# Performance work log

Measured on AMD Instinct MI355X. Metric: run time of the kernel, lower is better.

## Reference

```python
import jax, jax.numpy as jnp
import numpy as np

B, T, I, H, C = 256, 2048, 64, 32, 2


def setup_inputs() -> dict:
    key = jax.random.key(0)
    ks = jax.random.split(key, 12)
    s = 0.1
    return {
        "values": jax.random.normal(ks[0], (B, T, I), dtype=jnp.float32),
        "masks": (jax.random.uniform(ks[1], (B, T, I)) > 0.5).astype(jnp.float32),
        "deltas": jax.random.uniform(ks[2], (B, T, I), dtype=jnp.float32),
        # TemporalDecay linear: input_size -> rnn_hidden_size
        "W_decay": jax.random.normal(ks[3], (H, I), dtype=jnp.float32) * s,
        "b_decay": jax.random.normal(ks[4], (H,), dtype=jnp.float32) * s,
        "W_reg": jax.random.normal(ks[5], (I, H), dtype=jnp.float32) * s,
        "b_reg": jax.random.normal(ks[6], (I,), dtype=jnp.float32) * s,
        # LSTMCell: input 2*I, hidden H; gate order i,f,g,o (PyTorch)
        "W_ih": jax.random.normal(ks[7], (4 * H, 2 * I), dtype=jnp.float32) * s,
        "b_ih": jax.random.normal(ks[8], (4 * H,), dtype=jnp.float32) * s,
        "W_hh": jax.random.normal(ks[9], (4 * H, H), dtype=jnp.float32) * s,
        "b_hh": jax.random.normal(ks[10], (4 * H,), dtype=jnp.float32) * s,
        # output head: hidden -> n_classes
        "W_out": jax.random.normal(ks[11], (C, H), dtype=jnp.float32) * s,
        "b_out": jnp.zeros((C,), dtype=jnp.float32),
    }


def reference(values, masks, deltas, W_decay, b_decay, W_reg, b_reg,
              W_ih, b_ih, W_hh, b_hh, W_out, b_out):
    batch = values.shape[0]
    hid = W_decay.shape[0]

    def step(carry, xs):
        h, c = carry
        x, m, d = xs  # each [B, I]
        # gamma = exp(-relu(W d + b)); decay hidden state
        gamma = jnp.exp(-jax.nn.relu(d @ W_decay.T + b_decay))
        h = h * gamma
        x_h = h @ W_reg.T + b_reg
        x_c = m * x + (1.0 - m) * x_h
        inp = jnp.concatenate([x_c, m], axis=1)  # [B, 2I]
        gates = inp @ W_ih.T + b_ih + h @ W_hh.T + b_hh  # [B, 4H]
        i_g, f_g, g_g, o_g = jnp.split(gates, 4, axis=1)
        i_g = jax.nn.sigmoid(i_g)
        f_g = jax.nn.sigmoid(f_g)
        g_g = jnp.tanh(g_g)
        o_g = jax.nn.sigmoid(o_g)
        c_new = f_g * c + i_g * g_g
        h_new = o_g * jnp.tanh(c_new)
        return (h_new, c_new), x_c

    h0 = jnp.zeros((batch, hid), dtype=values.dtype)
    c0 = jnp.zeros((batch, hid), dtype=values.dtype)
    xs = (jnp.swapaxes(values, 0, 1), jnp.swapaxes(masks, 0, 1), jnp.swapaxes(deltas, 0, 1))
    (h, c), x_cs = jax.lax.scan(step, (h0, c0), xs)
    imputations = jnp.swapaxes(x_cs, 0, 1)  # [B, T, I]
    y_h = h @ W_out.T + b_out  # [B, C]
    return y_h, imputations
```

## Files before the change

kernel.cpp:

```cpp
#include <hip/hip_runtime.h>
#include <stdint.h>

#define L2E 1.4426950408889634f

typedef __attribute__((ext_vector_type(8))) short short8;
typedef __attribute__((ext_vector_type(4))) float floatx4;
typedef __attribute__((ext_vector_type(4))) unsigned int uintx4;
typedef __attribute__((ext_vector_type(2))) _Float16 half2v;

__device__ __forceinline__ uint32_t pkbf(float lo, float hi) {
  uint32_t r;
  asm("v_cvt_pk_bf16_f32 %0, %1, %2" : "=v"(r) : "v"(lo), "v"(hi));
  return r;
}
__device__ __forceinline__ uint32_t pkh(float lo, float hi) {
  uint32_t r;
  asm("v_cvt_pkrtz_f16_f32 %0, %1, %2" : "=v"(r) : "v"(lo), "v"(hi));
  return r;
}
__device__ __forceinline__ float2 uph(uint32_t u) {
  union { uint32_t u; half2v h; } z; z.u = u;
  return make_float2((float)z.h.x, (float)z.h.y);
}
__device__ __forceinline__ short8 mkfrag(const float* p) {
  float4 a = *(const float4*)p;
  float4 b = *(const float4*)(p + 4);
  union { uint32_t u[4]; short8 s; } z;
  z.u[0] = pkbf(a.x, a.y); z.u[1] = pkbf(a.z, a.w);
  z.u[2] = pkbf(b.x, b.y); z.u[3] = pkbf(b.z, b.w);
  return z.s;
}
__device__ __forceinline__ short8 pk8(float4 a, float4 b) {
  union { uint32_t u[4]; short8 s; } z;
  z.u[0] = pkbf(a.x, a.y); z.u[1] = pkbf(a.z, a.w);
  z.u[2] = pkbf(b.x, b.y); z.u[3] = pkbf(b.z, b.w);
  return z.s;
}
__device__ __forceinline__ short8 u4s8(uint32_t a, uint32_t b, uint32_t c, uint32_t d) {
  union { uint32_t u[4]; short8 s; } z;
  z.u[0] = a; z.u[1] = b; z.u[2] = c; z.u[3] = d;
  return z.s;
}

#define SWAP32(a, b) asm("v_permlane32_swap_b32 %0, %1" : "+v"(a), "+v"(b))
#define SWAP16(a, b) asm("v_permlane16_swap_b32 %0, %1" : "+v"(a), "+v"(b))

__global__ __launch_bounds__(256) void g1_pre(
    const float* __restrict__ values, const float* __restrict__ masks,
    const float* __restrict__ W_ih, const float* __restrict__ b_ih,
    const float* __restrict__ b_hh, uint2* __restrict__ pregS,
    uint2* __restrict__ mxS, float* __restrict__ m1S, int gstride)
{
  const int tid = threadIdx.x, wv = tid >> 6, l = tid & 63;
  const int c = l & 15, kw = l >> 4;
  const int tch = blockIdx.x, gr = blockIdx.y;
  const int tbase = tch * 8;

  short8 WF[8][4];
  #pragma unroll
  for (int tg = 0; tg < 8; ++tg)
    #pragma unroll
    for (int kc = 0; kc < 4; ++kc)
      WF[tg][kc] = mkfrag(W_ih + (size_t)(16*tg + c)*128 + 32*kc + 8*kw);

  float4 bias[8];
  #pragma unroll
  for (int tg = 0; tg < 8; ++tg) {
    float4 bi = *(const float4*)(b_ih + 16*tg + 4*kw);
    float4 bh = *(const float4*)(b_hh + 16*tg + 4*kw);
    bias[tg] = make_float4(bi.x+bh.x, bi.y+bh.y, bi.z+bh.z, bi.w+bh.w);
  }

  #pragma unroll 1
  for (int tt = 0; tt < 2; ++tt) {
    const int rec = tbase + wv*2 + tt;
    const size_t ibase = ((size_t)(gr*16 + c)*2048 + rec)*64;
    const float* xr = values + ibase;
    const float* mr = masks + ibase;
    float4 xa0 = *(const float4*)(xr + 8*kw),      xa1 = *(const float4*)(xr + 8*kw + 4);
    float4 xb0 = *(const float4*)(xr + 32 + 8*kw), xb1 = *(const float4*)(xr + 32 + 8*kw + 4);
    float4 ma0 = *(const float4*)(mr + 8*kw),      ma1 = *(const float4*)(mr + 8*kw + 4);
    float4 mb0 = *(const float4*)(mr + 32 + 8*kw), mb1 = *(const float4*)(mr + 32 + 8*kw + 4);
    float4 fa0 = make_float4(xa0.x*ma0.x, xa0.y*ma0.y, xa0.z*ma0.z, xa0.w*ma0.w);
    float4 fa1 = make_float4(xa1.x*ma1.x, xa1.y*ma1.y, xa1.z*ma1.z, xa1.w*ma1.w);
    float4 fb0 = make_float4(xb0.x*mb0.x, xb0.y*mb0.y, xb0.z*mb0.z, xb0.w*mb0.w);
    float4 fb1 = make_float4(xb1.x*mb1.x, xb1.y*mb1.y, xb1.z*mb1.z, xb1.w*mb1.w);

    short8 BF0 = pk8(fa0, fa1), BF1 = pk8(fb0, fb1);
    short8 BF2 = pk8(ma0, ma1), BF3 = pk8(mb0, mb1);

    floatx4 acc[8];
    #pragma unroll
    for (int tg = 0; tg < 8; ++tg) acc[tg] = (floatx4){0.f, 0.f, 0.f, 0.f};
    #pragma unroll
    for (int tg = 0; tg < 8; ++tg) {
      acc[tg] = __builtin_amdgcn_mfma_f32_16x16x32_bf16(WF[tg][0], BF0, acc[tg], 0, 0, 0);
      acc[tg] = __builtin_amdgcn_mfma_f32_16x16x32_bf16(WF[tg][1], BF1, acc[tg], 0, 0, 0);
      acc[tg] = __builtin_amdgcn_mfma_f32_16x16x32_bf16(WF[tg][2], BF2, acc[tg], 0, 0, 0);
      acc[tg] = __builtin_amdgcn_mfma_f32_16x16x32_bf16(WF[tg][3], BF3, acc[tg], 0, 0, 0);
    }

    uint2* pf = pregS + (size_t)(gr*gstride + rec)*512 + (c + 16*kw);
    #pragma unroll
    for (int tg = 0; tg < 8; ++tg)
      pf[tg*64] = make_uint2(pkh(acc[tg][0]+bias[tg].x, acc[tg][1]+bias[tg].y),
                             pkh(acc[tg][2]+bias[tg].z, acc[tg][3]+bias[tg].w));

    uint2* mx2 = mxS + (size_t)(gr*gstride + rec)*256;
    mx2[(2*kw+0)*16 + c] = make_uint2(pkh(fa0.x,fa0.y), pkh(fa0.z,fa0.w));
    mx2[(2*kw+1)*16 + c] = make_uint2(pkh(fa1.x,fa1.y), pkh(fa1.z,fa1.w));
    mx2[(8+2*kw)*16 + c] = make_uint2(pkh(fb0.x,fb0.y), pkh(fb0.z,fb0.w));
    mx2[(9+2*kw)*16 + c] = make_uint2(pkh(fb1.x,fb1.y), pkh(fb1.z,fb1.w));

    float4* m14 = (float4*)m1S + (size_t)(gr*gstride + rec)*256;
    m14[(2*kw+0)*16 + c] = make_float4(1.f-ma0.x, 1.f-ma0.y, 1.f-ma0.z, 1.f-ma0.w);
    m14[(2*kw+1)*16 + c] = make_float4(1.f-ma1.x, 1.f-ma1.y, 1.f-ma1.z, 1.f-ma1.w);
    m14[(8+2*kw)*16 + c] = make_float4(1.f-mb0.x, 1.f-mb0.y, 1.f-mb0.z, 1.f-mb0.w);
    m14[(9+2*kw)*16 + c] = make_float4(1.f-mb1.x, 1.f-mb1.y, 1.f-mb1.z, 1.f-mb1.w);
  }
}

__global__ __launch_bounds__(256) void g2_gam(
    const float* __restrict__ deltas, const float* __restrict__ W_decay,
    const float* __restrict__ b_decay, float* __restrict__ gamS, int gstride)
{
  const int tid = threadIdx.x, wv = tid >> 6, l = tid & 63;
  const int c = l & 15, kw = l >> 4;
  const int tch = blockIdx.x, gr = blockIdx.y;
  const int tbase = tch * 8;

  short8 AF[2][2];
  #pragma unroll
  for (int jt = 0; jt < 2; ++jt)
    #pragma unroll
    for (int kc = 0; kc < 2; ++kc)
      AF[jt][kc] = mkfrag(W_decay + (size_t)(16*jt + c)*64 + 32*kc + 8*kw);
  float4 bd0 = *(const float4*)(b_decay + 4*kw);
  float4 bd1 = *(const float4*)(b_decay + 16 + 4*kw);

  #pragma unroll 1
  for (int tt = 0; tt < 2; ++tt) {
    const int rec = tbase + wv*2 + tt;
    const float* dr = deltas + ((size_t)(gr*16 + c)*2048 + rec)*64;
    float4 da0 = *(const float4*)(dr + 8*kw),      da1 = *(const float4*)(dr + 8*kw + 4);
    float4 db0 = *(const float4*)(dr + 32 + 8*kw), db1 = *(const float4*)(dr + 32 + 8*kw + 4);
    short8 B0 = pk8(da0, da1), B1 = pk8(db0, db1);
    floatx4 zz = (floatx4){0.f, 0.f, 0.f, 0.f};
    floatx4 a0 = __builtin_amdgcn_mfma_f32_16x16x32_bf16(AF[0][0], B0, zz, 0, 0, 0);
    a0 = __builtin_amdgcn_mfma_f32_16x16x32_bf16(AF[0][1], B1, a0, 0, 0, 0);
    floatx4 a1 = __builtin_amdgcn_mfma_f32_16x16x32_bf16(AF[1][0], B0, zz, 0, 0, 0);
    a1 = __builtin_amdgcn_mfma_f32_16x16x32_bf16(AF[1][1], B1, a1, 0, 0, 0);
    float g0 = __builtin_amdgcn_exp2f(-fmaxf(a0[0]+bd0.x, 0.f) * L2E);
    float g1 = __builtin_amdgcn_exp2f(-fmaxf(a0[1]+bd0.y, 0.f) * L2E);
    float g2 = __builtin_amdgcn_exp2f(-fmaxf(a0[2]+bd0.z, 0.f) * L2E);
    float g3 = __builtin_amdgcn_exp2f(-fmaxf(a0[3]+bd0.w, 0.f) * L2E);
    float h0 = __builtin_amdgcn_exp2f(-fmaxf(a1[0]+bd1.x, 0.f) * L2E);
    float h1 = __builtin_amdgcn_exp2f(-fmaxf(a1[1]+bd1.y, 0.f) * L2E);
    float h2 = __builtin_amdgcn_exp2f(-fmaxf(a1[2]+bd1.z, 0.f) * L2E);
    float h3 = __builtin_amdgcn_exp2f(-fmaxf(a1[3]+bd1.w, 0.f) * L2E);
    uintx4 o = (uintx4){pkh(g0, g1), pkh(g2, g3), pkh(h0, h1), pkh(h2, h3)};
    ((uintx4*)gamS)[(size_t)(gr*gstride + rec)*64 + c + 16*kw] = o;
  }
}

#define PW(GI, GF, GG, GO, CC, HH) do { \
  float _si = __builtin_amdgcn_rcpf(1.f + __builtin_amdgcn_exp2f((GI) * -L2E)); \
  float _sf = __builtin_amdgcn_rcpf(1.f + __builtin_amdgcn_exp2f((GF) * -L2E)); \
  float _so = __builtin_amdgcn_rcpf(1.f + __builtin_amdgcn_exp2f((GO) * -L2E)); \
  float _tg = 1.f - 2.f*__builtin_amdgcn_rcpf(1.f + __builtin_amdgcn_exp2f((GG) * (2.f*L2E))); \
  float _cn = fmaf(_sf, (CC), _si*_tg); \
  float _tc = 1.f - 2.f*__builtin_amdgcn_rcpf(1.f + __builtin_amdgcn_exp2f(_cn * (2.f*L2E))); \
  (CC) = _cn; (HH) = _so * _tc; \
} while (0)

__global__ __launch_bounds__(128, 1) void p13_rnn(
    const float* __restrict__ W_hh, const float* __restrict__ W_reg,
    const float* __restrict__ W_ih, const float* __restrict__ b_reg,
    const float* __restrict__ W_out, const float* __restrict__ b_out,
    const uint2* __restrict__ pregS, const char* __restrict__ gamS,
    const float* __restrict__ m1S, char* __restrict__ hdG,
    float* __restrict__ y, int gstride)
{
  const int tid = threadIdx.x, gr = blockIdx.x;
  const int wid = tid >> 6, l = tid & 63;
  const int b = l & 15, w = l >> 4;

  __shared__ __align__(16) char hdB[2 * 1536];
  __shared__ float yL[2][16][2];

  short8 WhhA[4], WxcA0[4], WxcA1[4], WregA[4];
  #pragma unroll
  for (int tt = 0; tt < 4; ++tt) {
    const int tg = 2*tt + wid;
    WhhA[tt]  = mkfrag(W_hh + (size_t)(16*tg + b)*32 + 8*w);
    WxcA0[tt] = mkfrag(W_ih + (size_t)(16*tg + b)*128 + 8*w);
    WxcA1[tt] = mkfrag(W_ih + (size_t)(16*tg + b)*128 + 32 + 8*w);
    WregA[tt] = mkfrag(W_reg + (size_t)(16*tt + b)*32 + 8*w);
  }
  floatx4 brC[4];
  #pragma unroll
  for (int t = 0; t < 4; ++t) {
    float4 v = *(const float4*)(b_reg + 16*t + 4*w);
    brC[t] = (floatx4){v.x, v.y, v.z, v.w};
  }

  float4 h = make_float4(0.f, 0.f, 0.f, 0.f);
  float4 cv = make_float4(0.f, 0.f, 0.f, 0.f);

  const uint2* pPreg = pregS + (size_t)gr*gstride*512 + l;
  const char*  gamB  = gamS + (size_t)gr*gstride*1024 + (size_t)(b + 16*w)*16 + wid*8;
  const float4* pM1  = (const float4*)m1S + (size_t)gr*gstride*256;
  char* hdP = hdG + (size_t)gr*gstride*1024 + b*64 + wid*32 + w*8;

  uint2 PR[2][4], GM[2];
  float4 M1r[2][4];

  auto PREF = [&](int s, int j) {
    #pragma unroll
    for (int tt = 0; tt < 4; ++tt) PR[j][tt] = pPreg[(size_t)s*512 + (2*tt + wid)*64];
    GM[j] = *(const uint2*)(gamB + (size_t)s*1024);
    #pragma unroll
    for (int t = 0; t < 4; ++t) M1r[j][t] = pM1[(size_t)s*256 + (4*t + w)*16 + b];
  };

  auto BODY = [&](int j, int par) {
    float2 g01 = uph(GM[j].x), g23 = uph(GM[j].y);
    float4 hd = make_float4(h.x*g01.x, h.y*g01.y, h.z*g23.x, h.w*g23.y);
    uint32_t K0 = pkbf(hd.x, hd.y), K1 = pkbf(hd.z, hd.w);
    uint32_t S0 = K0, S1 = K1;
    *(uint2*)hdP = make_uint2(S0, S1);
    hdP += 1024;
    *(uint2*)(hdB + par*1536 + b*96 + wid*32 + w*8) = make_uint2(K0, K1);
    asm volatile("s_waitcnt lgkmcnt(0)" ::: "memory");
    __builtin_amdgcn_s_barrier();
    asm volatile("" ::: "memory");
    short8 Bhd = *(const short8*)(hdB + par*1536 + b*96 + w*16);

    floatx4 uu[4];
    #pragma unroll
    for (int t = 0; t < 4; ++t)
      uu[t] = __builtin_amdgcn_mfma_f32_16x16x32_bf16(WregA[t], Bhd, brC[t], 0, 0, 0);
    floatx4 ga[4];
    #pragma unroll
    for (int tt = 0; tt < 4; ++tt) {
      float2 p01 = uph(PR[j][tt].x), p23 = uph(PR[j][tt].y);
      floatx4 ci = {p01.x, p01.y, p23.x, p23.y};
      ga[tt] = __builtin_amdgcn_mfma_f32_16x16x32_bf16(WhhA[tt], Bhd, ci, 0, 0, 0);
    }

    uint32_t U[8];
    #pragma unroll
    for (int t = 0; t < 4; ++t) {
      float4 m1v = M1r[j][t];
      float v0 = m1v.x*uu[t][0], v1 = m1v.y*uu[t][1];
      float v2 = m1v.z*uu[t][2], v3 = m1v.w*uu[t][3];
      U[2*t]   = pkbf(v0, v1);
      U[2*t+1] = pkbf(v2, v3);
    }
    SWAP32(U[0], U[2]); SWAP32(U[1], U[3]);
    SWAP16(U[0], U[2]); SWAP16(U[1], U[3]);
    short8 Bv0 = u4s8(U[0], U[1], U[2], U[3]);
    SWAP32(U[4], U[6]); SWAP32(U[5], U[7]);
    SWAP16(U[4], U[6]); SWAP16(U[5], U[7]);
    short8 Bv1 = u4s8(U[4], U[5], U[6], U[7]);

    #pragma unroll
    for (int tt = 0; tt < 4; ++tt)
      ga[tt] = __builtin_amdgcn_mfma_f32_16x16x32_bf16(WxcA0[tt], Bv0, ga[tt], 0, 0, 0);
    #pragma unroll
    for (int tt = 0; tt < 4; ++tt)
      ga[tt] = __builtin_amdgcn_mfma_f32_16x16x32_bf16(WxcA1[tt], Bv1, ga[tt], 0, 0, 0);

    PW(ga[0][0], ga[1][0], ga[2][0], ga[3][0], cv.x, h.x);
    PW(ga[0][1], ga[1][1], ga[2][1], ga[3][1], cv.y, h.y);
    PW(ga[0][2], ga[1][2], ga[2][2], ga[3][2], cv.z, h.z);
    PW(ga[0][3], ga[1][3], ga[2][3], ga[3][3], cv.w, h.w);
  };

  PREF(0, 0); PREF(1, 1);
  #pragma unroll 1
  for (int s = 0; s < 2048; s += 2) {
    BODY(0, 0); PREF(s + 2, 0);
    BODY(1, 1); PREF(s + 3, 1);
  }

  {
    auto d4 = [](float4 a, float4 bb) {
      return fmaf(a.x, bb.x, fmaf(a.y, bb.y, fmaf(a.z, bb.z, a.w*bb.w)));
    };
    float4 wo0 = *(const float4*)(W_out + wid*16 + 4*w);
    float4 wo1 = *(const float4*)(W_out + 32 + wid*16 + 4*w);
    float p0 = d4(h, wo0);
    float p1 = d4(h, wo1);
    p0 += __shfl_xor(p0, 16); p0 += __shfl_xor(p0, 32);
    p1 += __shfl_xor(p1, 16); p1 += __shfl_xor(p1, 32);
    if (l < 16) { yL[wid][l][0] = p0; yL[wid][l][1] = p1; }
    asm volatile("s_waitcnt lgkmcnt(0)" ::: "memory");
    __builtin_amdgcn_s_barrier();
    asm volatile("" ::: "memory");
    if (wid == 0 && l < 16) {
      y[(gr*16 + l)*2 + 0] = yL[0][l][0] + yL[1][l][0] + b_out[0];
      y[(gr*16 + l)*2 + 1] = yL[0][l][1] + yL[1][l][1] + b_out[1];
    }
  }
}

__global__ __launch_bounds__(256) void p13_post(
    const float* __restrict__ W_reg, const float* __restrict__ b_reg,
    const char* __restrict__ hdG, const uint2* __restrict__ mxS,
    const float* __restrict__ m1S, float* __restrict__ imp, int gstride)
{
  const int tid = threadIdx.x, wv = tid >> 6, l = tid & 63;
  const int c = l & 15, kw = l >> 4;
  const int tch = blockIdx.x, gr = blockIdx.y;
  const int tbase = tch * 8;

  short8 WA[4];
  #pragma unroll
  for (int t = 0; t < 4; ++t)
    WA[t] = mkfrag(W_reg + (size_t)(16*t + c)*32 + 8*kw);
  floatx4 brC[4];
  #pragma unroll
  for (int t = 0; t < 4; ++t) {
    float4 v = *(const float4*)(b_reg + 16*t + 4*kw);
    brC[t] = (floatx4){v.x, v.y, v.z, v.w};
  }

  #pragma unroll 1
  for (int tt = 0; tt < 2; ++tt) {
    const int rec = tbase + wv*2 + tt;
    short8 Bhd = *(const short8*)(hdG + (size_t)(gr*gstride + rec)*1024 + c*64 + kw*16);
    floatx4 uu[4];
    #pragma unroll
    for (int t = 0; t < 4; ++t)
      uu[t] = __builtin_amdgcn_mfma_f32_16x16x32_bf16(WA[t], Bhd, brC[t], 0, 0, 0);

    float* dst = imp + ((size_t)(gr*16 + c)*2048 + rec)*64 + 4*kw;
    #pragma unroll
    for (int t = 0; t < 4; ++t) {
      float4 m1v = ((const float4*)m1S)[(size_t)(gr*gstride + rec)*256 + (4*t + kw)*16 + c];
      uint2 mxv = mxS[(size_t)(gr*gstride + rec)*256 + (4*t + kw)*16 + c];
      float2 mxa = uph(mxv.x), mxb = uph(mxv.y);
      *(float4*)(dst + 16*t) = make_float4(
          fmaf(m1v.x, uu[t][0], mxa.x), fmaf(m1v.y, uu[t][1], mxa.y),
          fmaf(m1v.z, uu[t][2], mxb.x), fmaf(m1v.w, uu[t][3], mxb.y));
    }
  }
}

extern "C" void kernel_launch(void* const* d_in, const int* in_sizes, int n_in,
                              void* d_out, int out_size, void* d_ws, size_t ws_size,
                              hipStream_t stream) {
  (void)in_sizes; (void)n_in; (void)out_size; (void)ws_size;
  const float* values  = (const float*)d_in[0];
  const float* masks   = (const float*)d_in[1];
  const float* deltas  = (const float*)d_in[2];
  const float* W_decay = (const float*)d_in[3];
  const float* b_decay = (const float*)d_in[4];
  const float* W_reg   = (const float*)d_in[5];
  const float* b_reg   = (const float*)d_in[6];
  const float* W_ih    = (const float*)d_in[7];
  const float* b_ih    = (const float*)d_in[8];
  const float* W_hh    = (const float*)d_in[9];
  const float* b_hh    = (const float*)d_in[10];
  const float* W_out   = (const float*)d_in[11];
  const float* b_out   = (const float*)d_in[12];
  float* y   = (float*)d_out;
  float* imp = (float*)d_out + 512;

  const int gstride = 2056;
  char* pregS = (char*)d_ws;
  char* gamS  = pregS + (size_t)16*gstride*4096;
  char* mxS   = gamS  + (size_t)16*gstride*1024;
  char* m1S   = mxS   + (size_t)16*gstride*2048;
  char* hdG   = m1S   + (size_t)16*gstride*4096;

  hipLaunchKernelGGL(g1_pre, dim3(256, 16), dim3(256), 0, stream,
                     values, masks, W_ih, b_ih, b_hh,
                     (uint2*)pregS, (uint2*)mxS, (float*)m1S, gstride);
  hipLaunchKernelGGL(g2_gam, dim3(256, 16), dim3(256), 0, stream,
                     deltas, W_decay, b_decay, (float*)gamS, gstride);
  hipLaunchKernelGGL(p13_rnn, dim3(16), dim3(128), 0, stream,
                     W_hh, W_reg, W_ih, b_reg, W_out, b_out,
                     (const uint2*)pregS, gamS, (const float*)m1S, hdG, y, gstride);
  hipLaunchKernelGGL(p13_post, dim3(256, 16), dim3(256), 0, stream,
                     W_reg, b_reg, hdG, (const uint2*)mxS, (const float*)m1S,
                     imp, gstride);
}
```

Measured before the change: 1.614 ms.

## Stage recurrent per-step inputs through an LDS ring via async global-to-LDS loads

The serial RNN kernel now prefetches each timestep's precomputed gate pre-activations, mask products and decay factors three steps ahead. It uses global_load_lds into a 4-slot shared-memory ring instead of loading them straight into registers two steps ahead. Per-wave vmcnt waits plus the existing per-step barrier ensure each slot has landed before it is read back from LDS one step ahead. The aim is to hide global memory latency on the latency-bound recurrence and free registers, at the cost of extra LDS traffic, about 37 KB of shared memory, and delicate wait-count bookkeeping.

```diff
diff --git a/kernel.cpp b/kernel.cpp
--- a/kernel.cpp
+++ b/kernel.cpp
@@ -44,6 +44,9 @@
 
 #define SWAP32(a, b) asm("v_permlane32_swap_b32 %0, %1" : "+v"(a), "+v"(b))
 #define SWAP16(a, b) asm("v_permlane16_swap_b32 %0, %1" : "+v"(a), "+v"(b))
+#define GLDS16(gp, lp) __builtin_amdgcn_global_load_lds( \
+    (const __attribute__((address_space(1))) void*)(gp), \
+    (__attribute__((address_space(3))) void*)(lp), 16, 0, 0)
 
 __global__ __launch_bounds__(256) void g1_pre(
     const float* __restrict__ values, const float* __restrict__ masks,
@@ -173,18 +176,21 @@
   (CC) = _cn; (HH) = _so * _tc; \
 } while (0)
 
-__global__ __launch_bounds__(128, 1) void p13_rnn(
+#define SLOTB 9216
+
+__global__ __launch_bounds__(128, 1) void p14_rnn(
     const float* __restrict__ W_hh, const float* __restrict__ W_reg,
     const float* __restrict__ W_ih, const float* __restrict__ b_reg,
     const float* __restrict__ W_out, const float* __restrict__ b_out,
-    const uint2* __restrict__ pregS, const char* __restrict__ gamS,
-    const float* __restrict__ m1S, char* __restrict__ hdG,
+    const char* __restrict__ pregS, const char* __restrict__ gamS,
+    const char* __restrict__ m1S, char* __restrict__ hdG,
     float* __restrict__ y, int gstride)
 {
   const int tid = threadIdx.x, gr = blockIdx.x;
   const int wid = tid >> 6, l = tid & 63;
   const int b = l & 15, w = l >> 4;
 
+  __shared__ __align__(16) char ring[4 * SLOTB];
   __shared__ __align__(16) char hdB[2 * 1536];
   __shared__ float yL[2][16][2];
 
@@ -207,34 +213,59 @@
   float4 h = make_float4(0.f, 0.f, 0.f, 0.f);
   float4 cv = make_float4(0.f, 0.f, 0.f, 0.f);
 
-  const uint2* pPreg = pregS + (size_t)gr*gstride*512 + l;
-  const char*  gamB  = gamS + (size_t)gr*gstride*1024 + (size_t)(b + 16*w)*16 + wid*8;
-  const float4* pM1  = (const float4*)m1S + (size_t)gr*gstride*256;
+  const char* pregB = pregS + (size_t)gr*gstride*4096 + (size_t)l*16;
+  const char* gamGB = gamS  + (size_t)gr*gstride*1024 + (size_t)l*16;
+  const char* m1B   = m1S   + (size_t)gr*gstride*4096 + (size_t)l*16;
   char* hdP = hdG + (size_t)gr*gstride*1024 + b*64 + wid*32 + w*8;
 
-  uint2 PR[2][4], GM[2];
+  auto PREFL = [&](int rec, int slot) {
+    char* sb = ring + slot * SLOTB;
+    const char* pb = pregB + (size_t)rec*4096;
+    const char* mb = m1B   + (size_t)rec*4096;
+    if (wid == 0) {
+      GLDS16(pb,        sb);
+      GLDS16(pb + 1024, sb + 1024);
+      GLDS16(pb + 2048, sb + 2048);
+      GLDS16(pb + 3072, sb + 3072);
+      GLDS16(mb,        sb + 4096);
+    } else {
+      GLDS16(mb + 1024, sb + 5120);
+      GLDS16(mb + 2048, sb + 6144);
+      GLDS16(mb + 3072, sb + 7168);
+      GLDS16(gamGB + (size_t)rec*1024, sb + 8192);
+    }
+  };
+
+  uint2 PRr[2][4], GMr[2];
   float4 M1r[2][4];
 
-  auto PREF = [&](int s, int j) {
-    #pragma unroll
-    for (int tt = 0; tt < 4; ++tt) PR[j][tt] = pPreg[(size_t)s*512 + (2*tt + wid)*64];
-    GM[j] = *(const uint2*)(gamB + (size_t)s*1024);
-    #pragma unroll
-    for (int t = 0; t < 4; ++t) M1r[j][t] = pM1[(size_t)s*256 + (4*t + w)*16 + b];
+  auto LDSRD = [&](int slot, int j) {
+    const char* sb = ring + slot * SLOTB;
+    #pragma unroll
+    for (int tt = 0; tt < 4; ++tt)
+      PRr[j][tt] = *(const uint2*)(sb + ((2*tt + wid)*64 + l)*8);
+    GMr[j] = *(const uint2*)(sb + 8192 + (b + 16*w)*16 + wid*8);
+    #pragma unroll
+    for (int t = 0; t < 4; ++t)
+      M1r[j][t] = *(const float4*)(sb + 4096 + ((4*t + w)*16 + b)*16);
   };
 
-  auto BODY = [&](int j, int par) {
-    float2 g01 = uph(GM[j].x), g23 = uph(GM[j].y);
+  auto BODY = [&](int s, int j, int par) {
+    PREFL(s + 3, (s + 3) & 3);
+    if (wid == 0) asm volatile("s_waitcnt vmcnt(12)" ::: "memory");
+    else          asm volatile("s_waitcnt vmcnt(10)" ::: "memory");
+
+    float2 g01 = uph(GMr[j].x), g23 = uph(GMr[j].y);
     float4 hd = make_float4(h.x*g01.x, h.y*g01.y, h.z*g23.x, h.w*g23.y);
     uint32_t K0 = pkbf(hd.x, hd.y), K1 = pkbf(hd.z, hd.w);
-    uint32_t S0 = K0, S1 = K1;
-    *(uint2*)hdP = make_uint2(S0, S1);
+    *(uint2*)hdP = make_uint2(K0, K1);
     hdP += 1024;
     *(uint2*)(hdB + par*1536 + b*96 + wid*32 + w*8) = make_uint2(K0, K1);
     asm volatile("s_waitcnt lgkmcnt(0)" ::: "memory");
     __builtin_amdgcn_s_barrier();
     asm volatile("" ::: "memory");
     short8 Bhd = *(const short8*)(hdB + par*1536 + b*96 + w*16);
+    LDSRD((s + 1) & 3, j ^ 1);
 
     floatx4 uu[4];
     #pragma unroll
@@ -243,7 +274,7 @@
     floatx4 ga[4];
     #pragma unroll
     for (int tt = 0; tt < 4; ++tt) {
-      float2 p01 = uph(PR[j][tt].x), p23 = uph(PR[j][tt].y);
+      float2 p01 = uph(PRr[j][tt].x), p23 = uph(PRr[j][tt].y);
       floatx4 ci = {p01.x, p01.y, p23.x, p23.y};
       ga[tt] = __builtin_amdgcn_mfma_f32_16x16x32_bf16(WhhA[tt], Bhd, ci, 0, 0, 0);
     }
@@ -277,11 +308,16 @@
     PW(ga[0][3], ga[1][3], ga[2][3], ga[3][3], cv.w, h.w);
   };
 
-  PREF(0, 0); PREF(1, 1);
+  PREFL(0, 0); PREFL(1, 1); PREFL(2, 2);
+  asm volatile("s_waitcnt vmcnt(0)" ::: "memory");
+  __builtin_amdgcn_s_barrier();
+  asm volatile("" ::: "memory");
+  LDSRD(0, 0);
+
   #pragma unroll 1
   for (int s = 0; s < 2048; s += 2) {
-    BODY(0, 0); PREF(s + 2, 0);
-    BODY(1, 1); PREF(s + 3, 1);
+    BODY(s, 0, 0);
+    BODY(s + 1, 1, 1);
   }
 
   {
@@ -380,9 +416,9 @@
                      (uint2*)pregS, (uint2*)mxS, (float*)m1S, gstride);
   hipLaunchKernelGGL(g2_gam, dim3(256, 16), dim3(256), 0, stream,
                      deltas, W_decay, b_decay, (float*)gamS, gstride);
-  hipLaunchKernelGGL(p13_rnn, dim3(16), dim3(128), 0, stream,
+  hipLaunchKernelGGL(p14_rnn, dim3(16), dim3(128), 0, stream,
                      W_hh, W_reg, W_ih, b_reg, W_out, b_out,
-                     (const uint2*)pregS, gamS, (const float*)m1S, hdG, y, gstride);
+                     pregS, gamS, m1S, hdG, y, gstride);
   hipLaunchKernelGGL(p13_post, dim3(256, 16), dim3(256), 0, stream,
                      W_reg, b_reg, hdG, (const uint2*)mxS, (const float*)m1S,
                      imp, gstride);
```

Measured after the change: 2.485 ms. 1.54x slower.
